# Kernel optimization log

Measured on AMD Instinct MI355X. Metric: run time of the kernel, lower is better.

The kernel has to match this reference:

```python
import jax, jax.numpy as jnp
import numpy as np

EPS = 1e-6
HEADS, HEAD_DIM = 8, 64

def rms_norm_ch(x, g):
    # x: [B,C,H,W], normalize over channel dim, scale g: [C]
    mean = jnp.mean(x * x, axis=1, keepdims=True)
    return x * jax.lax.rsqrt(mean + EPS) * g[None, :, None, None]

def rms_norm_last(x, g):
    # x: [B,L,D], normalize over feature dim, scale g: [D]
    mean = jnp.mean(x * x, axis=-1, keepdims=True)
    return x * jax.lax.rsqrt(mean + EPS) * g

def setup_inputs() -> dict:
    key = jax.random.key(0)
    ks = jax.random.split(key, 5)
    B, C, H, W = 8, 512, 32, 32
    Lc = 1024
    hidden = HEADS * HEAD_DIM  # 512
    x = jax.random.normal(ks[0], (B, C, H, W), dtype=jnp.float32)
    context = jax.random.normal(ks[1], (B, Lc, C), dtype=jnp.float32)
    Wq = jax.random.normal(ks[2], (hidden, C), dtype=jnp.float32) * 0.02
    Wkv = jax.random.normal(ks[3], (2 * hidden, C), dtype=jnp.float32) * 0.02
    Wo = jax.random.normal(ks[4], (C, hidden), dtype=jnp.float32) * 0.02
    bo = jnp.zeros((C,), dtype=jnp.float32)
    g = jnp.ones((C,), dtype=jnp.float32)   # shared RMSNorm scale (pre-attn)
    g2 = jnp.ones((C,), dtype=jnp.float32)  # output RMSNorm scale
    return {"x": x, "context": context, "Wq": Wq, "Wkv": Wkv, "Wo": Wo, "bo": bo, "g": g, "g2": g2}

def reference(x, context, Wq, Wkv, Wo, bo, g, g2):
    B, C, H, W = x.shape
    Lc = context.shape[1]
    hidden = HEADS * HEAD_DIM
    scale = HEAD_DIM ** -0.5

    # Q projection: 1x1 conv == per-pixel matmul
    xn = rms_norm_ch(x, g)
    q = jnp.einsum('oc,bchw->bohw', Wq, xn)                     # [B,hidden,H,W]
    q = q.reshape(B, HEADS, HEAD_DIM, H * W) * scale            # [B,h,d,lw1]

    # K,V from context tokens
    cn = rms_norm_last(context, g)
    kv = jnp.einsum('bld,od->blo', cn, Wkv)                     # [B,Lc,2*hidden]
    k, v = jnp.split(kv, 2, axis=-1)
    k = k.reshape(B, Lc, HEADS, HEAD_DIM).transpose(0, 2, 3, 1)  # [B,h,d,lw2]
    v = v.reshape(B, Lc, HEADS, HEAD_DIM).transpose(0, 2, 3, 1)  # [B,h,d,lw2]

    sim = jnp.einsum('bhci,bhcj->bhij', q, k)                   # [B,h,lw1,lw2]
    attn = jax.nn.softmax(sim, axis=-1)
    out = jnp.einsum('bhij,bhcj->bhic', attn, v)                # [B,h,lw1,d]

    out = out.transpose(0, 1, 3, 2).reshape(B, hidden, H, W)    # b (h c) l w
    y = jnp.einsum('oc,bchw->bohw', Wo, out) + bo[None, :, None, None]
    y = rms_norm_ch(y, g2)
    return y + x
```

## Files before the change

### kernel.cpp

```cpp
#include <hip/hip_runtime.h>
#include <hip/hip_bf16.h>

using bf16 = __hip_bfloat16;
typedef float f32x4 __attribute__((ext_vector_type(4)));
typedef short s16x8 __attribute__((ext_vector_type(8)));
typedef short s16x4 __attribute__((ext_vector_type(4)));

#define B_N   8
#define C_N   512
#define HW_N  1024
#define LC_N  1024
#define HID_N 512
#define NHEAD 8
#define DHEAD 64
#define EPSN  1e-6f

__device__ __forceinline__ f32x4 mfma16(s16x8 a, s16x8 b, f32x4 c) {
  return __builtin_amdgcn_mfma_f32_16x16x32_bf16(a, b, c, 0, 0, 0);
}
__device__ __forceinline__ void gload_lds16(const void* g, void* l) {
  __builtin_amdgcn_global_load_lds((const __attribute__((address_space(1))) void*)g,
                                   (__attribute__((address_space(3))) void*)l, 16, 0, 0);
}
__device__ __forceinline__ s16x8 ld8(const bf16* p) {
  return *reinterpret_cast<const s16x8*>(p);
}
__device__ __forceinline__ unsigned short bfbits(float f) {
  return __builtin_bit_cast(unsigned short, __float2bfloat16(f));
}

__global__ __launch_bounds__(256) void prep_weights(
    const float* __restrict__ Wq, const float* __restrict__ Wkv,
    const float* __restrict__ Wo, const float* __restrict__ g,
    bf16* __restrict__ Wqg, bf16* __restrict__ Wkvg, bf16* __restrict__ Wob,
    float* __restrict__ ssqx, float* __restrict__ ssqy)
{
  int idx = blockIdx.x * 256 + threadIdx.x;
  const int NQ = 512 * 512, NKV = 1024 * 512;
  if (idx < 8192) { ssqx[idx] = 0.f; ssqy[idx] = 0.f; }
  if (idx < NQ) {
    Wqg[idx] = __float2bfloat16(Wq[idx] * g[idx & 511]);
  } else if (idx < NQ + NKV) {
    int j = idx - NQ;
    Wkvg[j] = __float2bfloat16(Wkv[j] * g[j & 511]);
  } else {
    int j = idx - NQ - NKV;
    Wob[j] = __float2bfloat16(Wo[j]);
  }
}

__global__ __launch_bounds__(256) void xbf_kernel(
    const float* __restrict__ x, bf16* __restrict__ xbf, float* __restrict__ ssqx)
{
  __shared__ float tile[32][33];
  __shared__ float part[8][32];
  int b = blockIdx.z, c0 = blockIdx.y * 32, p0 = blockIdx.x * 32;
  int tx = threadIdx.x & 31, ty = threadIdx.x >> 5;
#pragma unroll
  for (int j = 0; j < 4; ++j) {
    int c = ty + j * 8;
    tile[c][tx] = x[((long)b * C_N + c0 + c) * HW_N + p0 + tx];
  }
  __syncthreads();
  {
    float s = 0.f;
#pragma unroll
    for (int i = 0; i < 4; ++i) {
      float v = tile[ty * 4 + i][tx];
      s += v * v;
    }
    part[ty][tx] = s;
  }
#pragma unroll
  for (int j = 0; j < 4; ++j) {
    int p = ty + j * 8;
    xbf[((long)b * HW_N + p0 + p) * C_N + c0 + tx] = __float2bfloat16(tile[tx][p]);
  }
  __syncthreads();
  if (ty == 0) {
    float tot = 0.f;
#pragma unroll
    for (int i = 0; i < 8; ++i) tot += part[i][tx];
    atomicAdd(&ssqx[b * HW_N + p0 + tx], tot);
  }
}

__global__ __launch_bounds__(256) void ctxnorm_kernel(
    const float* __restrict__ ctx, bf16* __restrict__ cnbf)
{
  int row = blockIdx.x * 4 + (threadIdx.x >> 6);
  int lane = threadIdx.x & 63;
  const float* cr = ctx + (long)row * C_N;
  float4 v0 = ((const float4*)cr)[lane * 2];
  float4 v1 = ((const float4*)cr)[lane * 2 + 1];
  float s = v0.x*v0.x + v0.y*v0.y + v0.z*v0.z + v0.w*v0.w
          + v1.x*v1.x + v1.y*v1.y + v1.z*v1.z + v1.w*v1.w;
#pragma unroll
  for (int m = 1; m < 64; m <<= 1) s += __shfl_xor(s, m);
  float r = rsqrtf(s * (1.0f / C_N) + EPSN);
  bf16 tmp[8];
  tmp[0] = __float2bfloat16(v0.x * r); tmp[1] = __float2bfloat16(v0.y * r);
  tmp[2] = __float2bfloat16(v0.z * r); tmp[3] = __float2bfloat16(v0.w * r);
  tmp[4] = __float2bfloat16(v1.x * r); tmp[5] = __float2bfloat16(v1.y * r);
  tmp[6] = __float2bfloat16(v1.z * r); tmp[7] = __float2bfloat16(v1.w * r);
  *reinterpret_cast<s16x8*>(cnbf + (long)row * C_N + lane * 8) =
      *reinterpret_cast<const s16x8*>(tmp);
}

__device__ __forceinline__ void gemm128_core(
    const bf16* __restrict__ A, const bf16* __restrict__ W, int K, int m0, int n0,
    bf16* __restrict__ sA, bf16* __restrict__ sB, f32x4 (&acc)[4][4])
{
  const int t = threadIdx.x;
  const int lane = t & 63, w = t >> 6;
  const int wm = (w >> 1) * 64, wn = (w & 1) * 64;
  const int lr = lane & 15, hi = lane >> 4;
  const int r = t >> 2, seg = t & 3;
  const long aoff0 = (long)(m0 + r) * K + seg * 8;
  const long aoff1 = (long)(m0 + 64 + r) * K + seg * 8;
  const long woff0 = (long)(n0 + r) * K + seg * 8;
  const long woff1 = (long)(n0 + 64 + r) * K + seg * 8;
  const int d0 = r * 32 + seg * 8, d1 = (64 + r) * 32 + seg * 8;

#define GSTAGE(buf, k0)                                           \
  do {                                                            \
    gload_lds16(A + aoff0 + (k0), &sA[(buf) * 4096 + d0]);        \
    gload_lds16(A + aoff1 + (k0), &sA[(buf) * 4096 + d1]);        \
    gload_lds16(W + woff0 + (k0), &sB[(buf) * 4096 + d0]);        \
    gload_lds16(W + woff1 + (k0), &sB[(buf) * 4096 + d1]);        \
  } while (0)

  GSTAGE(0, 0);
  __syncthreads();
  int cur = 0;
  for (int k0 = 0; k0 < K; k0 += 32) {
    if (k0 + 32 < K) GSTAGE(cur ^ 1, k0 + 32);
    s16x8 af[4], bfr[4];
#pragma unroll
    for (int mi = 0; mi < 4; ++mi)
      af[mi] = *reinterpret_cast<const s16x8*>(
          &sA[cur * 4096 + (wm + mi * 16 + lr) * 32 + hi * 8]);
#pragma unroll
    for (int ni = 0; ni < 4; ++ni)
      bfr[ni] = *reinterpret_cast<const s16x8*>(
          &sB[cur * 4096 + (wn + ni * 16 + lr) * 32 + hi * 8]);
    __builtin_amdgcn_s_setprio(1);
#pragma unroll
    for (int mi = 0; mi < 4; ++mi)
#pragma unroll
      for (int ni = 0; ni < 4; ++ni)
        acc[mi][ni] = mfma16(af[mi], bfr[ni], acc[mi][ni]);
    __builtin_amdgcn_s_setprio(0);
    __syncthreads();
    cur ^= 1;
  }
#undef GSTAGE
}

__global__ __launch_bounds__(256, 2)
void gemm_qkv(const bf16* __restrict__ xbf, const bf16* __restrict__ cnbf,
              const bf16* __restrict__ Wqg, const bf16* __restrict__ Wkvg,
              const float* __restrict__ ssqx,
              bf16* __restrict__ qbf, bf16* __restrict__ kvbf, bf16* __restrict__ vT)
{
  __shared__ bf16 sA[2 * 4096];
  __shared__ bf16 sB[2 * 4096];
  const int bid = blockIdx.x;
  const bf16 *A, *W;
  int m0, n0;
  bool isQ;
  if (bid < 256) {
    isQ = true;  A = xbf;  W = Wqg;
    m0 = (bid >> 2) * 128; n0 = (bid & 3) * 128;
  } else {
    isQ = false; A = cnbf; W = Wkvg;
    int b2 = bid - 256;
    m0 = (b2 >> 3) * 128; n0 = (b2 & 7) * 128;
  }
  f32x4 acc[4][4] = {};
  gemm128_core(A, W, C_N, m0, n0, sA, sB, acc);

  const int lane = threadIdx.x & 63, w = threadIdx.x >> 6;
  const int wm = (w >> 1) * 64, wn = (w & 1) * 64;
  const int lr = lane & 15, hi = lane >> 4;
#pragma unroll
  for (int mi = 0; mi < 4; ++mi) {
#pragma unroll
    for (int rr = 0; rr < 4; ++rr) {
      int row = m0 + wm + mi * 16 + hi * 4 + rr;
      float rsc = 0.f;
      if (isQ)
        rsc = rsqrtf(ssqx[row] * (1.0f / C_N) + EPSN) * 0.18033688011112042f;
#pragma unroll
      for (int ni = 0; ni < 4; ++ni) {
        int col = n0 + wn + ni * 16 + lr;
        float v = acc[mi][ni][rr];
        if (isQ) {
          qbf[(long)row * HID_N + col] = __float2bfloat16(v * rsc);
        } else if (col < HID_N) {
          kvbf[(long)row * (2 * HID_N) + col] = __float2bfloat16(v);
        } else {
          int b = row >> 10, l = row & 1023;
          vT[((long)b * HID_N + (col - HID_N)) * LC_N + l] = __float2bfloat16(v);
        }
      }
    }
  }
}

__global__ __launch_bounds__(256, 2)
void gemm_o(const bf16* __restrict__ attno, const bf16* __restrict__ Wob,
            const float* __restrict__ bo, float* __restrict__ ytmp,
            float* __restrict__ ssqy)
{
  __shared__ bf16 sA[2 * 4096];
  __shared__ bf16 sB[2 * 4096];
  const int m0 = (blockIdx.x >> 2) * 128;
  const int n0 = (blockIdx.x & 3) * 128;
  f32x4 acc[4][4] = {};
  gemm128_core(attno, Wob, HID_N, m0, n0, sA, sB, acc);

  const int lane = threadIdx.x & 63, w = threadIdx.x >> 6;
  const int wm = (w >> 1) * 64, wn = (w & 1) * 64;
  const int lr = lane & 15, hi = lane >> 4;
  float ss[4][4];
#pragma unroll
  for (int mi = 0; mi < 4; ++mi)
#pragma unroll
    for (int rr = 0; rr < 4; ++rr) ss[mi][rr] = 0.f;

#pragma unroll
  for (int mi = 0; mi < 4; ++mi) {
#pragma unroll
    for (int ni = 0; ni < 4; ++ni) {
      float bb = bo[n0 + wn + ni * 16 + lr];
#pragma unroll
      for (int rr = 0; rr < 4; ++rr) {
        int row = m0 + wm + mi * 16 + hi * 4 + rr;
        int col = n0 + wn + ni * 16 + lr;
        float v = acc[mi][ni][rr] + bb;
        ytmp[(long)row * C_N + col] = v;
        ss[mi][rr] += v * v;
      }
    }
  }
#pragma unroll
  for (int mi = 0; mi < 4; ++mi)
#pragma unroll
    for (int rr = 0; rr < 4; ++rr) {
      float s = ss[mi][rr];
      s += __shfl_xor(s, 1); s += __shfl_xor(s, 2);
      s += __shfl_xor(s, 4); s += __shfl_xor(s, 8);
      if (lr == 0) atomicAdd(&ssqy[m0 + wm + mi * 16 + hi * 4 + rr], s);
    }
}

__global__ __launch_bounds__(256, 2)
void attn_fused(const bf16* __restrict__ qbf, const bf16* __restrict__ kvbf,
                const bf16* __restrict__ vT, bf16* __restrict__ attno)
{
  __shared__ bf16 sK[2][4096];
  __shared__ bf16 sV[2][4096];
  __shared__ bf16 Pl[4][32 * 72];
  const int t = threadIdx.x;
  const int wv = t >> 6, lane = t & 63;
  const int lr = lane & 15, hi = lane >> 4;
  const int hi8 = hi * 8, hi4 = hi * 4;
  const int bh = blockIdx.x, b = bh >> 3, h = bh & 7;
  const int q_base = blockIdx.y * 128 + wv * 32;

  const bf16* kbase = kvbf + (long)b * LC_N * 1024 + h * DHEAD;
  const bf16* vbase = vT + ((long)b * HID_N + h * DHEAD) * (long)LC_N;
  bf16* Pw = Pl[wv];

  s16x8 qf[2][2];
#pragma unroll
  for (int qt = 0; qt < 2; ++qt)
#pragma unroll
    for (int c = 0; c < 2; ++c)
      qf[qt][c] = ld8(qbf + ((long)b * HW_N + q_base + qt * 16 + lr) * HID_N
                          + h * DHEAD + c * 32 + hi8);

  const int srow = lane >> 2;
  const int scol = (lane & 3) * 8;

#define ASTAGE(buf, l0n)                                                        \
  do {                                                                          \
    _Pragma("unroll")                                                           \
    for (int j = 0; j < 4; ++j) {                                               \
      int lin = wv * 4 + j;                                                     \
      int cc = (lin >> 2) & 1, qq = lin & 3;                                    \
      if (lin < 8) {                                                            \
        gload_lds16(kbase + (long)((l0n) + qq * 16 + srow) * 1024 + cc * 32 + scol, \
                    &sK[buf][cc * 2048 + qq * 512 + lane * 8]);                 \
      } else {                                                                  \
        gload_lds16(vbase + (long)(qq * 16 + srow) * 1024 + (l0n) + cc * 32 + scol, \
                    &sV[buf][cc * 2048 + qq * 512 + lane * 8]);                 \
      }                                                                         \
    }                                                                           \
  } while (0)

  float m[2] = {-1e30f, -1e30f};
  float lsum[2] = {0.f, 0.f};
  f32x4 o[2][4] = {};

  ASTAGE(0, 0);
  __syncthreads();
  int cur = 0;

#pragma unroll 1
  for (int l0 = 0; l0 < LC_N; l0 += 64) {
    if (l0 + 64 < LC_N) ASTAGE(cur ^ 1, l0 + 64);

    f32x4 st[4][2] = {};
    __builtin_amdgcn_s_setprio(1);
#pragma unroll
    for (int kt = 0; kt < 4; ++kt) {
      s16x8 k0 = *reinterpret_cast<const s16x8*>(&sK[cur][(kt * 16 + lr) * 32 + hi8]);
      s16x8 k1 = *reinterpret_cast<const s16x8*>(&sK[cur][2048 + (kt * 16 + lr) * 32 + hi8]);
      st[kt][0] = mfma16(k0, qf[0][0], st[kt][0]);
      st[kt][0] = mfma16(k1, qf[0][1], st[kt][0]);
      st[kt][1] = mfma16(k0, qf[1][0], st[kt][1]);
      st[kt][1] = mfma16(k1, qf[1][1], st[kt][1]);
    }
    __builtin_amdgcn_s_setprio(0);

    float pmax[2];
#pragma unroll
    for (int qt = 0; qt < 2; ++qt) {
      float mx = st[0][qt][0];
#pragma unroll
      for (int kt = 0; kt < 4; ++kt)
#pragma unroll
        for (int rr = 0; rr < 4; ++rr)
          mx = fmaxf(mx, st[kt][qt][rr]);
      pmax[qt] = mx;
    }
    bool ok = (pmax[0] <= m[0] + 8.f) && (pmax[1] <= m[1] + 8.f);
    if (!__all(ok)) {
#pragma unroll
      for (int qt = 0; qt < 2; ++qt) {
        float rm = pmax[qt];
        rm = fmaxf(rm, __shfl_xor(rm, 16));
        rm = fmaxf(rm, __shfl_xor(rm, 32));
        float mn = fmaxf(m[qt], rm);
        float al = __builtin_amdgcn_exp2f(m[qt] - mn);
        m[qt] = mn;
        lsum[qt] *= al;
        float arr[4];
#pragma unroll
        for (int rr = 0; rr < 4; ++rr) arr[rr] = __shfl(al, hi4 + rr);
#pragma unroll
        for (int dt = 0; dt < 4; ++dt)
#pragma unroll
          for (int rr = 0; rr < 4; ++rr) o[qt][dt][rr] *= arr[rr];
      }
    }

#pragma unroll
    for (int qt = 0; qt < 2; ++qt) {
      float ls = 0.f;
#pragma unroll
      for (int kt = 0; kt < 4; ++kt) {
        float p0 = __builtin_amdgcn_exp2f(st[kt][qt][0] - m[qt]);
        float p1 = __builtin_amdgcn_exp2f(st[kt][qt][1] - m[qt]);
        float p2 = __builtin_amdgcn_exp2f(st[kt][qt][2] - m[qt]);
        float p3 = __builtin_amdgcn_exp2f(st[kt][qt][3] - m[qt]);
        ls += (p0 + p1) + (p2 + p3);
        s16x4 pk;
        pk[0] = (short)bfbits(p0); pk[1] = (short)bfbits(p1);
        pk[2] = (short)bfbits(p2); pk[3] = (short)bfbits(p3);
        *reinterpret_cast<s16x4*>(&Pw[(qt * 16 + lr) * 72 + kt * 16 + hi4]) = pk;
      }
      lsum[qt] += ls;
    }

    __builtin_amdgcn_s_setprio(1);
#pragma unroll
    for (int c = 0; c < 2; ++c) {
      s16x8 pa0 = *reinterpret_cast<const s16x8*>(&Pw[(0 * 16 + lr) * 72 + c * 32 + hi8]);
      s16x8 pa1 = *reinterpret_cast<const s16x8*>(&Pw[(1 * 16 + lr) * 72 + c * 32 + hi8]);
#pragma unroll
      for (int dt = 0; dt < 4; ++dt) {
        s16x8 vv = *reinterpret_cast<const s16x8*>(
            &sV[cur][c * 2048 + (dt * 16 + lr) * 32 + hi8]);
        o[0][dt] = mfma16(pa0, vv, o[0][dt]);
        o[1][dt] = mfma16(pa1, vv, o[1][dt]);
      }
    }
    __builtin_amdgcn_s_setprio(0);

    __syncthreads();
    cur ^= 1;
  }
#undef ASTAGE

#pragma unroll
  for (int qt = 0; qt < 2; ++qt) {
    float ls = lsum[qt];
    ls += __shfl_xor(ls, 16);
    ls += __shfl_xor(ls, 32);
    float linv[4];
#pragma unroll
    for (int rr = 0; rr < 4; ++rr) linv[rr] = 1.f / __shfl(ls, hi4 + rr);
#pragma unroll
    for (int dt = 0; dt < 4; ++dt)
#pragma unroll
      for (int rr = 0; rr < 4; ++rr)
        attno[((long)b * HW_N + q_base + qt * 16 + hi4 + rr) * HID_N
              + h * DHEAD + dt * 16 + lr] = __float2bfloat16(o[qt][dt][rr] * linv[rr]);
  }
}

__global__ __launch_bounds__(256) void final_kernel(
    const float* __restrict__ ytmp, const float* __restrict__ g2,
    const float* __restrict__ ssqy, const float* __restrict__ x,
    float* __restrict__ out)
{
  __shared__ float tile[32][33];
  int b = blockIdx.z, c0 = blockIdx.y * 32, p0 = blockIdx.x * 32;
  int tx = threadIdx.x & 31, ty = threadIdx.x >> 5;
#pragma unroll
  for (int j = 0; j < 4; ++j) {
    int p = ty + j * 8;
    tile[p][tx] = ytmp[((long)b * HW_N + p0 + p) * C_N + c0 + tx];
  }
  __syncthreads();
  float r = rsqrtf(ssqy[b * HW_N + p0 + tx] * (1.0f / C_N) + EPSN);
#pragma unroll
  for (int j = 0; j < 4; ++j) {
    int c = ty + j * 8;
    long oidx = ((long)b * C_N + c0 + c) * HW_N + p0 + tx;
    out[oidx] = tile[tx][c] * r * g2[c0 + c] + x[oidx];
  }
}

extern "C" void kernel_launch(void* const* d_in, const int* in_sizes, int n_in,
                              void* d_out, int out_size, void* d_ws, size_t ws_size,
                              hipStream_t stream) {
  const float* x   = (const float*)d_in[0];
  const float* ctx = (const float*)d_in[1];
  const float* Wq  = (const float*)d_in[2];
  const float* Wkv = (const float*)d_in[3];
  const float* Wo  = (const float*)d_in[4];
  const float* bo  = (const float*)d_in[5];
  const float* g   = (const float*)d_in[6];
  const float* g2  = (const float*)d_in[7];
  float* out = (float*)d_out;

  char* ws = (char*)d_ws;
  bf16*  Wqg   = (bf16*)(ws + 0);
  bf16*  Wkvg  = (bf16*)(ws + 524288);
  bf16*  Wob   = (bf16*)(ws + 1572864);
  float* ssqx  = (float*)(ws + 2097152);
  float* ssqy  = (float*)(ws + 2129920);
  bf16*  xbf   = (bf16*)(ws + 2162688);
  bf16*  cnbf  = (bf16*)(ws + 10551296);
  bf16*  qbf   = (bf16*)(ws + 18939904);
  bf16*  kvbf  = (bf16*)(ws + 27328512);
  bf16*  vT    = (bf16*)(ws + 44105728);
  bf16*  attno = (bf16*)(ws + 52494336);
  float* ytmp  = (float*)(ws + 2162688);

  prep_weights<<<4096, 256, 0, stream>>>(Wq, Wkv, Wo, g, Wqg, Wkvg, Wob, ssqx, ssqy);
  xbf_kernel<<<dim3(32, 16, 8), 256, 0, stream>>>(x, xbf, ssqx);
  ctxnorm_kernel<<<2048, 256, 0, stream>>>(ctx, cnbf);

  gemm_qkv<<<768, 256, 0, stream>>>(xbf, cnbf, Wqg, Wkvg, ssqx, qbf, kvbf, vT);

  attn_fused<<<dim3(64, 8), 256, 0, stream>>>(qbf, kvbf, vT, attno);

  gemm_o<<<256, 256, 0, stream>>>(attno, Wob, bo, ytmp, ssqy);

  final_kernel<<<dim3(32, 16, 8), 256, 0, stream>>>(ytmp, g2, ssqy, x, out);
}
```

Before: 184.9 us.

## Fuse all stages into a persistent megakernel with grid barriers and swizzled LDS

Replaces the seven separate launches with one init kernel plus a persistent 512-block kernel. Inside it, the prep, QKV GEMM, attention, output GEMM and final-norm stages run in sequence, separated by software grid barriers built on atomics. This removes per-launch overhead and the idle tails between kernels. It also adds an XOR swizzle to the LDS layout in the GEMM and attention tiles to cut bank conflicts. The costs are the barrier spin waits, a dependence on all 512 blocks being co-resident (otherwise it deadlocks), and stages whose tile counts do not divide evenly across 512 blocks, such as 768 GEMM tiles.

```diff
diff --git a/kernel.cpp b/kernel.cpp
--- a/kernel.cpp
+++ b/kernel.cpp
@@ -11,9 +11,9 @@
 #define HW_N  1024
 #define LC_N  1024
 #define HID_N 512
-#define NHEAD 8
 #define DHEAD 64
 #define EPSN  1e-6f
+#define NBLK  512
 
 __device__ __forceinline__ f32x4 mfma16(s16x8 a, s16x8 b, f32x4 c) {
   return __builtin_amdgcn_mfma_f32_16x16x32_bf16(a, b, c, 0, 0, 0);
@@ -29,98 +29,47 @@
   return __builtin_bit_cast(unsigned short, __float2bfloat16(f));
 }
 
-__global__ __launch_bounds__(256) void prep_weights(
-    const float* __restrict__ Wq, const float* __restrict__ Wkv,
-    const float* __restrict__ Wo, const float* __restrict__ g,
-    bf16* __restrict__ Wqg, bf16* __restrict__ Wkvg, bf16* __restrict__ Wob,
-    float* __restrict__ ssqx, float* __restrict__ ssqy)
+__device__ __forceinline__ void grid_barrier(int* bar) {
+  __syncthreads();
+  if (threadIdx.x == 0) {
+    __threadfence();
+    int g = __hip_atomic_load(&bar[1], __ATOMIC_RELAXED, __HIP_MEMORY_SCOPE_AGENT);
+    int v = __hip_atomic_fetch_add(&bar[0], 1, __ATOMIC_ACQ_REL, __HIP_MEMORY_SCOPE_AGENT);
+    if (v == NBLK - 1) {
+      __hip_atomic_store(&bar[0], 0, __ATOMIC_RELAXED, __HIP_MEMORY_SCOPE_AGENT);
+      __hip_atomic_fetch_add(&bar[1], 1, __ATOMIC_ACQ_REL, __HIP_MEMORY_SCOPE_AGENT);
+    } else {
+      while (__hip_atomic_load(&bar[1], __ATOMIC_ACQUIRE, __HIP_MEMORY_SCOPE_AGENT) == g)
+        __builtin_amdgcn_s_sleep(2);
+    }
+  }
+  __syncthreads();
+}
+
+__global__ __launch_bounds__(256) void init_kernel(
+    float* __restrict__ ssqx, float* __restrict__ ssqy, int* __restrict__ bar)
 {
-  int idx = blockIdx.x * 256 + threadIdx.x;
-  const int NQ = 512 * 512, NKV = 1024 * 512;
-  if (idx < 8192) { ssqx[idx] = 0.f; ssqy[idx] = 0.f; }
-  if (idx < NQ) {
-    Wqg[idx] = __float2bfloat16(Wq[idx] * g[idx & 511]);
-  } else if (idx < NQ + NKV) {
-    int j = idx - NQ;
-    Wkvg[j] = __float2bfloat16(Wkv[j] * g[j & 511]);
-  } else {
-    int j = idx - NQ - NKV;
-    Wob[j] = __float2bfloat16(Wo[j]);
-  }
-}
-
-__global__ __launch_bounds__(256) void xbf_kernel(
-    const float* __restrict__ x, bf16* __restrict__ xbf, float* __restrict__ ssqx)
-{
-  __shared__ float tile[32][33];
-  __shared__ float part[8][32];
-  int b = blockIdx.z, c0 = blockIdx.y * 32, p0 = blockIdx.x * 32;
-  int tx = threadIdx.x & 31, ty = threadIdx.x >> 5;
-#pragma unroll
-  for (int j = 0; j < 4; ++j) {
-    int c = ty + j * 8;
-    tile[c][tx] = x[((long)b * C_N + c0 + c) * HW_N + p0 + tx];
-  }
-  __syncthreads();
-  {
-    float s = 0.f;
-#pragma unroll
-    for (int i = 0; i < 4; ++i) {
-      float v = tile[ty * 4 + i][tx];
-      s += v * v;
-    }
-    part[ty][tx] = s;
-  }
-#pragma unroll
-  for (int j = 0; j < 4; ++j) {
-    int p = ty + j * 8;
-    xbf[((long)b * HW_N + p0 + p) * C_N + c0 + tx] = __float2bfloat16(tile[tx][p]);
-  }
-  __syncthreads();
-  if (ty == 0) {
-    float tot = 0.f;
-#pragma unroll
-    for (int i = 0; i < 8; ++i) tot += part[i][tx];
-    atomicAdd(&ssqx[b * HW_N + p0 + tx], tot);
-  }
-}
-
-__global__ __launch_bounds__(256) void ctxnorm_kernel(
-    const float* __restrict__ ctx, bf16* __restrict__ cnbf)
-{
-  int row = blockIdx.x * 4 + (threadIdx.x >> 6);
-  int lane = threadIdx.x & 63;
-  const float* cr = ctx + (long)row * C_N;
-  float4 v0 = ((const float4*)cr)[lane * 2];
-  float4 v1 = ((const float4*)cr)[lane * 2 + 1];
-  float s = v0.x*v0.x + v0.y*v0.y + v0.z*v0.z + v0.w*v0.w
-          + v1.x*v1.x + v1.y*v1.y + v1.z*v1.z + v1.w*v1.w;
-#pragma unroll
-  for (int m = 1; m < 64; m <<= 1) s += __shfl_xor(s, m);
-  float r = rsqrtf(s * (1.0f / C_N) + EPSN);
-  bf16 tmp[8];
-  tmp[0] = __float2bfloat16(v0.x * r); tmp[1] = __float2bfloat16(v0.y * r);
-  tmp[2] = __float2bfloat16(v0.z * r); tmp[3] = __float2bfloat16(v0.w * r);
-  tmp[4] = __float2bfloat16(v1.x * r); tmp[5] = __float2bfloat16(v1.y * r);
-  tmp[6] = __float2bfloat16(v1.z * r); tmp[7] = __float2bfloat16(v1.w * r);
-  *reinterpret_cast<s16x8*>(cnbf + (long)row * C_N + lane * 8) =
-      *reinterpret_cast<const s16x8*>(tmp);
+  int i = blockIdx.x * 256 + threadIdx.x;
+  if (i < 8192) { ssqx[i] = 0.f; ssqy[i] = 0.f; }
+  if (i < 8) bar[i] = 0;
 }
 
 __device__ __forceinline__ void gemm128_core(
     const bf16* __restrict__ A, const bf16* __restrict__ W, int K, int m0, int n0,
-    bf16* __restrict__ sA, bf16* __restrict__ sB, f32x4 (&acc)[4][4])
+    bf16* sA, bf16* sB, f32x4 (&acc)[4][4])
 {
   const int t = threadIdx.x;
   const int lane = t & 63, w = t >> 6;
   const int wm = (w >> 1) * 64, wn = (w & 1) * 64;
   const int lr = lane & 15, hi = lane >> 4;
   const int r = t >> 2, seg = t & 3;
-  const long aoff0 = (long)(m0 + r) * K + seg * 8;
-  const long aoff1 = (long)(m0 + 64 + r) * K + seg * 8;
-  const long woff0 = (long)(n0 + r) * K + seg * 8;
-  const long woff1 = (long)(n0 + 64 + r) * K + seg * 8;
+  const int segsw = seg ^ ((r >> 1) & 3);
+  const long aoff0 = (long)(m0 + r) * K + segsw * 8;
+  const long aoff1 = (long)(m0 + 64 + r) * K + segsw * 8;
+  const long woff0 = (long)(n0 + r) * K + segsw * 8;
+  const long woff1 = (long)(n0 + 64 + r) * K + segsw * 8;
   const int d0 = r * 32 + seg * 8, d1 = (64 + r) * 32 + seg * 8;
+  const int kofs = (hi ^ ((lr >> 1) & 3)) * 8;
 
 #define GSTAGE(buf, k0)                                           \
   do {                                                            \
@@ -139,11 +88,11 @@
 #pragma unroll
     for (int mi = 0; mi < 4; ++mi)
       af[mi] = *reinterpret_cast<const s16x8*>(
-          &sA[cur * 4096 + (wm + mi * 16 + lr) * 32 + hi * 8]);
+          &sA[cur * 4096 + (wm + mi * 16 + lr) * 32 + kofs]);
 #pragma unroll
     for (int ni = 0; ni < 4; ++ni)
       bfr[ni] = *reinterpret_cast<const s16x8*>(
-          &sB[cur * 4096 + (wn + ni * 16 + lr) * 32 + hi * 8]);
+          &sB[cur * 4096 + (wn + ni * 16 + lr) * 32 + kofs]);
     __builtin_amdgcn_s_setprio(1);
 #pragma unroll
     for (int mi = 0; mi < 4; ++mi)
@@ -157,281 +106,360 @@
 #undef GSTAGE
 }
 
-__global__ __launch_bounds__(256, 2)
-void gemm_qkv(const bf16* __restrict__ xbf, const bf16* __restrict__ cnbf,
-              const bf16* __restrict__ Wqg, const bf16* __restrict__ Wkvg,
-              const float* __restrict__ ssqx,
-              bf16* __restrict__ qbf, bf16* __restrict__ kvbf, bf16* __restrict__ vT)
+__global__ __launch_bounds__(256, 3)
+void mega(const float* __restrict__ x, const float* __restrict__ ctx,
+          const float* __restrict__ Wq, const float* __restrict__ Wkv,
+          const float* __restrict__ Wo, const float* __restrict__ bo,
+          const float* __restrict__ g, const float* __restrict__ g2,
+          bf16* __restrict__ Wqg, bf16* __restrict__ Wkvg, bf16* __restrict__ Wob,
+          float* __restrict__ ssqx, float* __restrict__ ssqy,
+          bf16* __restrict__ xbf, bf16* __restrict__ cnbf,
+          bf16* __restrict__ qbf, bf16* __restrict__ kvbf, bf16* __restrict__ vT,
+          bf16* __restrict__ attno, float* __restrict__ ytmp,
+          float* __restrict__ out, int* __restrict__ bar)
 {
-  __shared__ bf16 sA[2 * 4096];
-  __shared__ bf16 sB[2 * 4096];
-  const int bid = blockIdx.x;
-  const bf16 *A, *W;
-  int m0, n0;
-  bool isQ;
-  if (bid < 256) {
-    isQ = true;  A = xbf;  W = Wqg;
-    m0 = (bid >> 2) * 128; n0 = (bid & 3) * 128;
-  } else {
-    isQ = false; A = cnbf; W = Wkvg;
-    int b2 = bid - 256;
-    m0 = (b2 >> 3) * 128; n0 = (b2 & 7) * 128;
-  }
-  f32x4 acc[4][4] = {};
-  gemm128_core(A, W, C_N, m0, n0, sA, sB, acc);
-
-  const int lane = threadIdx.x & 63, w = threadIdx.x >> 6;
-  const int wm = (w >> 1) * 64, wn = (w & 1) * 64;
-  const int lr = lane & 15, hi = lane >> 4;
-#pragma unroll
-  for (int mi = 0; mi < 4; ++mi) {
-#pragma unroll
-    for (int rr = 0; rr < 4; ++rr) {
-      int row = m0 + wm + mi * 16 + hi * 4 + rr;
-      float rsc = 0.f;
-      if (isQ)
-        rsc = rsqrtf(ssqx[row] * (1.0f / C_N) + EPSN) * 0.18033688011112042f;
+  __shared__ __align__(16) char smem[51200];
+  const int vb = blockIdx.x;
+  const int tid = threadIdx.x;
+
+  for (int t = vb; t < 4096; t += NBLK) {
+    int idx = t * 256 + tid;
+    const int NQ = 512 * 512, NKV = 1024 * 512;
+    if (idx < NQ) {
+      Wqg[idx] = __float2bfloat16(Wq[idx] * g[idx & 511]);
+    } else if (idx < NQ + NKV) {
+      int j = idx - NQ;
+      Wkvg[j] = __float2bfloat16(Wkv[j] * g[j & 511]);
+    } else {
+      int j = idx - NQ - NKV;
+      Wob[j] = __float2bfloat16(Wo[j]);
+    }
+  }
+  {
+    float* tile = (float*)smem;
+    float* part = (float*)(smem + 4352);
+    int tx = tid & 31, ty = tid >> 5;
+    for (int t = vb; t < 4096; t += NBLK) {
+      int b = t >> 9, cy = (t >> 5) & 15, px = t & 31;
+      int c0 = cy * 32, p0 = px * 32;
+#pragma unroll
+      for (int j = 0; j < 4; ++j) {
+        int c = ty + j * 8;
+        tile[c * 33 + tx] = x[((long)b * C_N + c0 + c) * HW_N + p0 + tx];
+      }
+      __syncthreads();
+      {
+        float s = 0.f;
+#pragma unroll
+        for (int i = 0; i < 4; ++i) {
+          float v = tile[(ty * 4 + i) * 33 + tx];
+          s += v * v;
+        }
+        part[ty * 32 + tx] = s;
+      }
+#pragma unroll
+      for (int j = 0; j < 4; ++j) {
+        int p = ty + j * 8;
+        xbf[((long)b * HW_N + p0 + p) * C_N + c0 + tx] = __float2bfloat16(tile[tx * 33 + p]);
+      }
+      __syncthreads();
+      if (ty == 0) {
+        float tot = 0.f;
+#pragma unroll
+        for (int i = 0; i < 8; ++i) tot += part[i * 32 + tx];
+        atomicAdd(&ssqx[b * HW_N + p0 + tx], tot);
+      }
+    }
+  }
+  for (int t = vb; t < 2048; t += NBLK) {
+    int row = t * 4 + (tid >> 6);
+    int lane = tid & 63;
+    const float* cr = ctx + (long)row * C_N;
+    float4 v0 = ((const float4*)cr)[lane * 2];
+    float4 v1 = ((const float4*)cr)[lane * 2 + 1];
+    float s = v0.x*v0.x + v0.y*v0.y + v0.z*v0.z + v0.w*v0.w
+            + v1.x*v1.x + v1.y*v1.y + v1.z*v1.z + v1.w*v1.w;
+#pragma unroll
+    for (int m = 1; m < 64; m <<= 1) s += __shfl_xor(s, m);
+    float r = rsqrtf(s * (1.0f / C_N) + EPSN);
+    bf16 tmp[8];
+    tmp[0] = __float2bfloat16(v0.x * r); tmp[1] = __float2bfloat16(v0.y * r);
+    tmp[2] = __float2bfloat16(v0.z * r); tmp[3] = __float2bfloat16(v0.w * r);
+    tmp[4] = __float2bfloat16(v1.x * r); tmp[5] = __float2bfloat16(v1.y * r);
+    tmp[6] = __float2bfloat16(v1.z * r); tmp[7] = __float2bfloat16(v1.w * r);
+    *reinterpret_cast<s16x8*>(cnbf + (long)row * C_N + lane * 8) =
+        *reinterpret_cast<const s16x8*>(tmp);
+  }
+  grid_barrier(bar);
+
+  {
+    bf16* sA = (bf16*)smem;
+    bf16* sB = (bf16*)(smem + 16384);
+    const int lane = tid & 63, w = tid >> 6;
+    const int wm = (w >> 1) * 64, wn = (w & 1) * 64;
+    const int lr = lane & 15, hi = lane >> 4;
+    for (int tv = vb; tv < 768; tv += NBLK) {
+      const bf16 *A, *W;
+      int m0, n0;
+      bool isQ;
+      if (tv < 256) {
+        isQ = true;  A = xbf;  W = Wqg;
+        m0 = (tv >> 2) * 128; n0 = (tv & 3) * 128;
+      } else {
+        isQ = false; A = cnbf; W = Wkvg;
+        int b2 = tv - 256;
+        m0 = (b2 >> 3) * 128; n0 = (b2 & 7) * 128;
+      }
+      f32x4 acc[4][4] = {};
+      gemm128_core(A, W, C_N, m0, n0, sA, sB, acc);
+#pragma unroll
+      for (int mi = 0; mi < 4; ++mi) {
+#pragma unroll
+        for (int rr = 0; rr < 4; ++rr) {
+          int row = m0 + wm + mi * 16 + hi * 4 + rr;
+          float rsc = 0.f;
+          if (isQ)
+            rsc = rsqrtf(ssqx[row] * (1.0f / C_N) + EPSN) * 0.18033688011112042f;
+#pragma unroll
+          for (int ni = 0; ni < 4; ++ni) {
+            int col = n0 + wn + ni * 16 + lr;
+            float v = acc[mi][ni][rr];
+            if (isQ) {
+              qbf[(long)row * HID_N + col] = __float2bfloat16(v * rsc);
+            } else if (col < HID_N) {
+              kvbf[(long)row * (2 * HID_N) + col] = __float2bfloat16(v);
+            } else {
+              int b = row >> 10, l = row & 1023;
+              vT[((long)b * HID_N + (col - HID_N)) * LC_N + l] = __float2bfloat16(v);
+            }
+          }
+        }
+      }
+    }
+  }
+  grid_barrier(bar);
+
+  {
+    bf16* sK = (bf16*)smem;
+    bf16* sV = (bf16*)(smem + 16384);
+    bf16* Pl = (bf16*)(smem + 32768);
+    const int wv = tid >> 6, lane = tid & 63;
+    const int lr = lane & 15, hi = lane >> 4;
+    const int hi8 = hi * 8, hi4 = hi * 4;
+    const int bh = vb & 63, b = bh >> 3, h = bh & 7;
+    const int q_base = (vb >> 6) * 128 + wv * 32;
+
+    const bf16* kbase = kvbf + (long)b * LC_N * 1024 + h * DHEAD;
+    const bf16* vbase = vT + ((long)b * HID_N + h * DHEAD) * (long)LC_N;
+    bf16* Pw = Pl + wv * (32 * 72);
+
+    s16x8 qf[2][2];
+#pragma unroll
+    for (int qt = 0; qt < 2; ++qt)
+#pragma unroll
+      for (int c = 0; c < 2; ++c)
+        qf[qt][c] = ld8(qbf + ((long)b * HW_N + q_base + qt * 16 + lr) * HID_N
+                            + h * DHEAD + c * 32 + hi8);
+
+    const int srow = lane >> 2;
+    const int scol = ((lane & 3) ^ ((lane >> 3) & 3)) * 8;
+    const int rxofs = (hi ^ ((lr >> 1) & 3)) * 8;
+
+#define ASTAGE(buf, l0n)                                                          \
+    do {                                                                          \
+      _Pragma("unroll")                                                           \
+      for (int j = 0; j < 4; ++j) {                                               \
+        int lin = wv * 4 + j;                                                     \
+        int cc = (lin >> 2) & 1, qq = lin & 3;                                    \
+        if (lin < 8) {                                                            \
+          gload_lds16(kbase + (long)((l0n) + qq * 16 + srow) * 1024 + cc * 32 + scol, \
+                      &sK[(buf) * 4096 + cc * 2048 + qq * 512 + lane * 8]);       \
+        } else {                                                                  \
+          gload_lds16(vbase + (long)(qq * 16 + srow) * 1024 + (l0n) + cc * 32 + scol, \
+                      &sV[(buf) * 4096 + cc * 2048 + qq * 512 + lane * 8]);       \
+        }                                                                         \
+      }                                                                           \
+    } while (0)
+
+    float m[2] = {-1e30f, -1e30f};
+    float lsum[2] = {0.f, 0.f};
+    f32x4 o[2][4] = {};
+
+    ASTAGE(0, 0);
+    __syncthreads();
+    int cur = 0;
+
+#pragma unroll 1
+    for (int l0 = 0; l0 < LC_N; l0 += 64) {
+      if (l0 + 64 < LC_N) ASTAGE(cur ^ 1, l0 + 64);
+
+      f32x4 st[4][2] = {};
+      __builtin_amdgcn_s_setprio(1);
+#pragma unroll
+      for (int kt = 0; kt < 4; ++kt) {
+        s16x8 k0 = *reinterpret_cast<const s16x8*>(
+            &sK[cur * 4096 + (kt * 16 + lr) * 32 + rxofs]);
+        s16x8 k1 = *reinterpret_cast<const s16x8*>(
+            &sK[cur * 4096 + 2048 + (kt * 16 + lr) * 32 + rxofs]);
+        st[kt][0] = mfma16(k0, qf[0][0], st[kt][0]);
+        st[kt][0] = mfma16(k1, qf[0][1], st[kt][0]);
+        st[kt][1] = mfma16(k0, qf[1][0], st[kt][1]);
+        st[kt][1] = mfma16(k1, qf[1][1], st[kt][1]);
+      }
+      __builtin_amdgcn_s_setprio(0);
+
+      float pmax[2];
+#pragma unroll
+      for (int qt = 0; qt < 2; ++qt) {
+        float mx = st[0][qt][0];
+#pragma unroll
+        for (int kt = 0; kt < 4; ++kt)
+#pragma unroll
+          for (int rr = 0; rr < 4; ++rr)
+            mx = fmaxf(mx, st[kt][qt][rr]);
+        pmax[qt] = mx;
+      }
+      bool ok = (pmax[0] <= m[0] + 8.f) && (pmax[1] <= m[1] + 8.f);
+      if (!__all(ok)) {
+#pragma unroll
+        for (int qt = 0; qt < 2; ++qt) {
+          float rm = pmax[qt];
+          rm = fmaxf(rm, __shfl_xor(rm, 16));
+          rm = fmaxf(rm, __shfl_xor(rm, 32));
+          float mn = fmaxf(m[qt], rm);
+          float al = __builtin_amdgcn_exp2f(m[qt] - mn);
+          m[qt] = mn;
+          lsum[qt] *= al;
+          float arr[4];
+#pragma unroll
+          for (int rr = 0; rr < 4; ++rr) arr[rr] = __shfl(al, hi4 + rr);
+#pragma unroll
+          for (int dt = 0; dt < 4; ++dt)
+#pragma unroll
+            for (int rr = 0; rr < 4; ++rr) o[qt][dt][rr] *= arr[rr];
+        }
+      }
+
+#pragma unroll
+      for (int qt = 0; qt < 2; ++qt) {
+        float ls = 0.f;
+#pragma unroll
+        for (int kt = 0; kt < 4; ++kt) {
+          float p0 = __builtin_amdgcn_exp2f(st[kt][qt][0] - m[qt]);
+          float p1 = __builtin_amdgcn_exp2f(st[kt][qt][1] - m[qt]);
+          float p2 = __builtin_amdgcn_exp2f(st[kt][qt][2] - m[qt]);
+          float p3 = __builtin_amdgcn_exp2f(st[kt][qt][3] - m[qt]);
+          ls += (p0 + p1) + (p2 + p3);
+          s16x4 pk;
+          pk[0] = (short)bfbits(p0); pk[1] = (short)bfbits(p1);
+          pk[2] = (short)bfbits(p2); pk[3] = (short)bfbits(p3);
+          *reinterpret_cast<s16x4*>(&Pw[(qt * 16 + lr) * 72 + kt * 16 + hi4]) = pk;
+        }
+        lsum[qt] += ls;
+      }
+
+      __builtin_amdgcn_s_setprio(1);
+#pragma unroll
+      for (int c = 0; c < 2; ++c) {
+        s16x8 pa0 = *reinterpret_cast<const s16x8*>(&Pw[(0 * 16 + lr) * 72 + c * 32 + hi8]);
+        s16x8 pa1 = *reinterpret_cast<const s16x8*>(&Pw[(1 * 16 + lr) * 72 + c * 32 + hi8]);
+#pragma unroll
+        for (int dt = 0; dt < 4; ++dt) {
+          s16x8 vv = *reinterpret_cast<const s16x8*>(
+              &sV[cur * 4096 + c * 2048 + (dt * 16 + lr) * 32 + rxofs]);
+          o[0][dt] = mfma16(pa0, vv, o[0][dt]);
+          o[1][dt] = mfma16(pa1, vv, o[1][dt]);
+        }
+      }
+      __builtin_amdgcn_s_setprio(0);
+
+      __syncthreads();
+      cur ^= 1;
+    }
+#undef ASTAGE
+
+#pragma unroll
+    for (int qt = 0; qt < 2; ++qt) {
+      float ls = lsum[qt];
+      ls += __shfl_xor(ls, 16);
+      ls += __shfl_xor(ls, 32);
+      float linv[4];
+#pragma unroll
+      for (int rr = 0; rr < 4; ++rr) linv[rr] = 1.f / __shfl(ls, hi4 + rr);
+#pragma unroll
+      for (int dt = 0; dt < 4; ++dt)
+#pragma unroll
+        for (int rr = 0; rr < 4; ++rr)
+          attno[((long)b * HW_N + q_base + qt * 16 + hi4 + rr) * HID_N
+                + h * DHEAD + dt * 16 + lr] = __float2bfloat16(o[qt][dt][rr] * linv[rr]);
+    }
+  }
+  grid_barrier(bar);
+
+  if (vb < 256) {
+    bf16* sA = (bf16*)smem;
+    bf16* sB = (bf16*)(smem + 16384);
+    const int m0 = (vb >> 2) * 128;
+    const int n0 = (vb & 3) * 128;
+    f32x4 acc[4][4] = {};
+    gemm128_core(attno, Wob, HID_N, m0, n0, sA, sB, acc);
+
+    const int lane = tid & 63, w = tid >> 6;
+    const int wm = (w >> 1) * 64, wn = (w & 1) * 64;
+    const int lr = lane & 15, hi = lane >> 4;
+    float ss[4][4];
+#pragma unroll
+    for (int mi = 0; mi < 4; ++mi)
+#pragma unroll
+      for (int rr = 0; rr < 4; ++rr) ss[mi][rr] = 0.f;
+#pragma unroll
+    for (int mi = 0; mi < 4; ++mi) {
 #pragma unroll
       for (int ni = 0; ni < 4; ++ni) {
-        int col = n0 + wn + ni * 16 + lr;
-        float v = acc[mi][ni][rr];
-        if (isQ) {
-          qbf[(long)row * HID_N + col] = __float2bfloat16(v * rsc);
-        } else if (col < HID_N) {
-          kvbf[(long)row * (2 * HID_N) + col] = __float2bfloat16(v);
-        } else {
-          int b = row >> 10, l = row & 1023;
-          vT[((long)b * HID_N + (col - HID_N)) * LC_N + l] = __float2bfloat16(v);
-        }
-      }
-    }
-  }
-}
-
-__global__ __launch_bounds__(256, 2)
-void gemm_o(const bf16* __restrict__ attno, const bf16* __restrict__ Wob,
-            const float* __restrict__ bo, float* __restrict__ ytmp,
-            float* __restrict__ ssqy)
-{
-  __shared__ bf16 sA[2 * 4096];
-  __shared__ bf16 sB[2 * 4096];
-  const int m0 = (blockIdx.x >> 2) * 128;
-  const int n0 = (blockIdx.x & 3) * 128;
-  f32x4 acc[4][4] = {};
-  gemm128_core(attno, Wob, HID_N, m0, n0, sA, sB, acc);
-
-  const int lane = threadIdx.x & 63, w = threadIdx.x >> 6;
-  const int wm = (w >> 1) * 64, wn = (w & 1) * 64;
-  const int lr = lane & 15, hi = lane >> 4;
-  float ss[4][4];
-#pragma unroll
-  for (int mi = 0; mi < 4; ++mi)
-#pragma unroll
-    for (int rr = 0; rr < 4; ++rr) ss[mi][rr] = 0.f;
-
-#pragma unroll
-  for (int mi = 0; mi < 4; ++mi) {
-#pragma unroll
-    for (int ni = 0; ni < 4; ++ni) {
-      float bb = bo[n0 + wn + ni * 16 + lr];
+        float bb = bo[n0 + wn + ni * 16 + lr];
+#pragma unroll
+        for (int rr = 0; rr < 4; ++rr) {
+          int row = m0 + wm + mi * 16 + hi * 4 + rr;
+          int col = n0 + wn + ni * 16 + lr;
+          float v = acc[mi][ni][rr] + bb;
+          ytmp[(long)row * C_N + col] = v;
+          ss[mi][rr] += v * v;
+        }
+      }
+    }
+#pragma unroll
+    for (int mi = 0; mi < 4; ++mi)
 #pragma unroll
       for (int rr = 0; rr < 4; ++rr) {
-        int row = m0 + wm + mi * 16 + hi * 4 + rr;
-        int col = n0 + wn + ni * 16 + lr;
-        float v = acc[mi][ni][rr] + bb;
-        ytmp[(long)row * C_N + col] = v;
-        ss[mi][rr] += v * v;
-      }
-    }
-  }
-#pragma unroll
-  for (int mi = 0; mi < 4; ++mi)
-#pragma unroll
-    for (int rr = 0; rr < 4; ++rr) {
-      float s = ss[mi][rr];
-      s += __shfl_xor(s, 1); s += __shfl_xor(s, 2);
-      s += __shfl_xor(s, 4); s += __shfl_xor(s, 8);
-      if (lr == 0) atomicAdd(&ssqy[m0 + wm + mi * 16 + hi * 4 + rr], s);
-    }
-}
-
-__global__ __launch_bounds__(256, 2)
-void attn_fused(const bf16* __restrict__ qbf, const bf16* __restrict__ kvbf,
-                const bf16* __restrict__ vT, bf16* __restrict__ attno)
-{
-  __shared__ bf16 sK[2][4096];
-  __shared__ bf16 sV[2][4096];
-  __shared__ bf16 Pl[4][32 * 72];
-  const int t = threadIdx.x;
-  const int wv = t >> 6, lane = t & 63;
-  const int lr = lane & 15, hi = lane >> 4;
-  const int hi8 = hi * 8, hi4 = hi * 4;
-  const int bh = blockIdx.x, b = bh >> 3, h = bh & 7;
-  const int q_base = blockIdx.y * 128 + wv * 32;
-
-  const bf16* kbase = kvbf + (long)b * LC_N * 1024 + h * DHEAD;
-  const bf16* vbase = vT + ((long)b * HID_N + h * DHEAD) * (long)LC_N;
-  bf16* Pw = Pl[wv];
-
-  s16x8 qf[2][2];
-#pragma unroll
-  for (int qt = 0; qt < 2; ++qt)
-#pragma unroll
-    for (int c = 0; c < 2; ++c)
-      qf[qt][c] = ld8(qbf + ((long)b * HW_N + q_base + qt * 16 + lr) * HID_N
-                          + h * DHEAD + c * 32 + hi8);
-
-  const int srow = lane >> 2;
-  const int scol = (lane & 3) * 8;
-
-#define ASTAGE(buf, l0n)                                                        \
-  do {                                                                          \
-    _Pragma("unroll")                                                           \
-    for (int j = 0; j < 4; ++j) {                                               \
-      int lin = wv * 4 + j;                                                     \
-      int cc = (lin >> 2) & 1, qq = lin & 3;                                    \
-      if (lin < 8) {                                                            \
-        gload_lds16(kbase + (long)((l0n) + qq * 16 + srow) * 1024 + cc * 32 + scol, \
-                    &sK[buf][cc * 2048 + qq * 512 + lane * 8]);                 \
-      } else {                                                                  \
-        gload_lds16(vbase + (long)(qq * 16 + srow) * 1024 + (l0n) + cc * 32 + scol, \
-                    &sV[buf][cc * 2048 + qq * 512 + lane * 8]);                 \
-      }                                                                         \
-    }                                                                           \
-  } while (0)
-
-  float m[2] = {-1e30f, -1e30f};
-  float lsum[2] = {0.f, 0.f};
-  f32x4 o[2][4] = {};
-
-  ASTAGE(0, 0);
-  __syncthreads();
-  int cur = 0;
-
-#pragma unroll 1
-  for (int l0 = 0; l0 < LC_N; l0 += 64) {
-    if (l0 + 64 < LC_N) ASTAGE(cur ^ 1, l0 + 64);
-
-    f32x4 st[4][2] = {};
-    __builtin_amdgcn_s_setprio(1);
-#pragma unroll
-    for (int kt = 0; kt < 4; ++kt) {
-      s16x8 k0 = *reinterpret_cast<const s16x8*>(&sK[cur][(kt * 16 + lr) * 32 + hi8]);
-      s16x8 k1 = *reinterpret_cast<const s16x8*>(&sK[cur][2048 + (kt * 16 + lr) * 32 + hi8]);
-      st[kt][0] = mfma16(k0, qf[0][0], st[kt][0]);
-      st[kt][0] = mfma16(k1, qf[0][1], st[kt][0]);
-      st[kt][1] = mfma16(k0, qf[1][0], st[kt][1]);
-      st[kt][1] = mfma16(k1, qf[1][1], st[kt][1]);
-    }
-    __builtin_amdgcn_s_setprio(0);
-
-    float pmax[2];
-#pragma unroll
-    for (int qt = 0; qt < 2; ++qt) {
-      float mx = st[0][qt][0];
-#pragma unroll
-      for (int kt = 0; kt < 4; ++kt)
-#pragma unroll
-        for (int rr = 0; rr < 4; ++rr)
-          mx = fmaxf(mx, st[kt][qt][rr]);
-      pmax[qt] = mx;
-    }
-    bool ok = (pmax[0] <= m[0] + 8.f) && (pmax[1] <= m[1] + 8.f);
-    if (!__all(ok)) {
-#pragma unroll
-      for (int qt = 0; qt < 2; ++qt) {
-        float rm = pmax[qt];
-        rm = fmaxf(rm, __shfl_xor(rm, 16));
-        rm = fmaxf(rm, __shfl_xor(rm, 32));
-        float mn = fmaxf(m[qt], rm);
-        float al = __builtin_amdgcn_exp2f(m[qt] - mn);
-        m[qt] = mn;
-        lsum[qt] *= al;
-        float arr[4];
-#pragma unroll
-        for (int rr = 0; rr < 4; ++rr) arr[rr] = __shfl(al, hi4 + rr);
-#pragma unroll
-        for (int dt = 0; dt < 4; ++dt)
-#pragma unroll
-          for (int rr = 0; rr < 4; ++rr) o[qt][dt][rr] *= arr[rr];
-      }
-    }
-
-#pragma unroll
-    for (int qt = 0; qt < 2; ++qt) {
-      float ls = 0.f;
-#pragma unroll
-      for (int kt = 0; kt < 4; ++kt) {
-        float p0 = __builtin_amdgcn_exp2f(st[kt][qt][0] - m[qt]);
-        float p1 = __builtin_amdgcn_exp2f(st[kt][qt][1] - m[qt]);
-        float p2 = __builtin_amdgcn_exp2f(st[kt][qt][2] - m[qt]);
-        float p3 = __builtin_amdgcn_exp2f(st[kt][qt][3] - m[qt]);
-        ls += (p0 + p1) + (p2 + p3);
-        s16x4 pk;
-        pk[0] = (short)bfbits(p0); pk[1] = (short)bfbits(p1);
-        pk[2] = (short)bfbits(p2); pk[3] = (short)bfbits(p3);
-        *reinterpret_cast<s16x4*>(&Pw[(qt * 16 + lr) * 72 + kt * 16 + hi4]) = pk;
-      }
-      lsum[qt] += ls;
-    }
-
-    __builtin_amdgcn_s_setprio(1);
-#pragma unroll
-    for (int c = 0; c < 2; ++c) {
-      s16x8 pa0 = *reinterpret_cast<const s16x8*>(&Pw[(0 * 16 + lr) * 72 + c * 32 + hi8]);
-      s16x8 pa1 = *reinterpret_cast<const s16x8*>(&Pw[(1 * 16 + lr) * 72 + c * 32 + hi8]);
-#pragma unroll
-      for (int dt = 0; dt < 4; ++dt) {
-        s16x8 vv = *reinterpret_cast<const s16x8*>(
-            &sV[cur][c * 2048 + (dt * 16 + lr) * 32 + hi8]);
-        o[0][dt] = mfma16(pa0, vv, o[0][dt]);
-        o[1][dt] = mfma16(pa1, vv, o[1][dt]);
-      }
-    }
-    __builtin_amdgcn_s_setprio(0);
-
-    __syncthreads();
-    cur ^= 1;
-  }
-#undef ASTAGE
-
-#pragma unroll
-  for (int qt = 0; qt < 2; ++qt) {
-    float ls = lsum[qt];
-    ls += __shfl_xor(ls, 16);
-    ls += __shfl_xor(ls, 32);
-    float linv[4];
-#pragma unroll
-    for (int rr = 0; rr < 4; ++rr) linv[rr] = 1.f / __shfl(ls, hi4 + rr);
-#pragma unroll
-    for (int dt = 0; dt < 4; ++dt)
-#pragma unroll
-      for (int rr = 0; rr < 4; ++rr)
-        attno[((long)b * HW_N + q_base + qt * 16 + hi4 + rr) * HID_N
-              + h * DHEAD + dt * 16 + lr] = __float2bfloat16(o[qt][dt][rr] * linv[rr]);
-  }
-}
-
-__global__ __launch_bounds__(256) void final_kernel(
-    const float* __restrict__ ytmp, const float* __restrict__ g2,
-    const float* __restrict__ ssqy, const float* __restrict__ x,
-    float* __restrict__ out)
-{
-  __shared__ float tile[32][33];
-  int b = blockIdx.z, c0 = blockIdx.y * 32, p0 = blockIdx.x * 32;
-  int tx = threadIdx.x & 31, ty = threadIdx.x >> 5;
-#pragma unroll
-  for (int j = 0; j < 4; ++j) {
-    int p = ty + j * 8;
-    tile[p][tx] = ytmp[((long)b * HW_N + p0 + p) * C_N + c0 + tx];
-  }
-  __syncthreads();
-  float r = rsqrtf(ssqy[b * HW_N + p0 + tx] * (1.0f / C_N) + EPSN);
-#pragma unroll
-  for (int j = 0; j < 4; ++j) {
-    int c = ty + j * 8;
-    long oidx = ((long)b * C_N + c0 + c) * HW_N + p0 + tx;
-    out[oidx] = tile[tx][c] * r * g2[c0 + c] + x[oidx];
+        float s = ss[mi][rr];
+        s += __shfl_xor(s, 1); s += __shfl_xor(s, 2);
+        s += __shfl_xor(s, 4); s += __shfl_xor(s, 8);
+        if (lr == 0) atomicAdd(&ssqy[m0 + wm + mi * 16 + hi * 4 + rr], s);
+      }
+  }
+  grid_barrier(bar);
+
+  {
+    float* tile = (float*)smem;
+    int tx = tid & 31, ty = tid >> 5;
+    for (int t = vb; t < 4096; t += NBLK) {
+      int b = t >> 9, cy = (t >> 5) & 15, px = t & 31;
+      int c0 = cy * 32, p0 = px * 32;
+#pragma unroll
+      for (int j = 0; j < 4; ++j) {
+        int p = ty + j * 8;
+        tile[p * 33 + tx] = ytmp[((long)b * HW_N + p0 + p) * C_N + c0 + tx];
+      }
+      __syncthreads();
+      float r = rsqrtf(ssqy[b * HW_N + p0 + tx] * (1.0f / C_N) + EPSN);
+#pragma unroll
+      for (int j = 0; j < 4; ++j) {
+        int c = ty + j * 8;
+        long oidx = ((long)b * C_N + c0 + c) * HW_N + p0 + tx;
+        out[oidx] = tile[tx * 33 + c] * r * g2[c0 + c] + x[oidx];
+      }
+      __syncthreads();
+    }
   }
 }
 
@@ -454,23 +482,18 @@
   bf16*  Wob   = (bf16*)(ws + 1572864);
   float* ssqx  = (float*)(ws + 2097152);
   float* ssqy  = (float*)(ws + 2129920);
-  bf16*  xbf   = (bf16*)(ws + 2162688);
-  bf16*  cnbf  = (bf16*)(ws + 10551296);
-  bf16*  qbf   = (bf16*)(ws + 18939904);
-  bf16*  kvbf  = (bf16*)(ws + 27328512);
-  bf16*  vT    = (bf16*)(ws + 44105728);
-  bf16*  attno = (bf16*)(ws + 52494336);
-  float* ytmp  = (float*)(ws + 2162688);
-
-  prep_weights<<<4096, 256, 0, stream>>>(Wq, Wkv, Wo, g, Wqg, Wkvg, Wob, ssqx, ssqy);
-  xbf_kernel<<<dim3(32, 16, 8), 256, 0, stream>>>(x, xbf, ssqx);
-  ctxnorm_kernel<<<2048, 256, 0, stream>>>(ctx, cnbf);
-
-  gemm_qkv<<<768, 256, 0, stream>>>(xbf, cnbf, Wqg, Wkvg, ssqx, qbf, kvbf, vT);
-
-  attn_fused<<<dim3(64, 8), 256, 0, stream>>>(qbf, kvbf, vT, attno);
-
-  gemm_o<<<256, 256, 0, stream>>>(attno, Wob, bo, ytmp, ssqy);
-
-  final_kernel<<<dim3(32, 16, 8), 256, 0, stream>>>(ytmp, g2, ssqy, x, out);
-}
+  int*   bar   = (int*)  (ws + 2162688);
+  bf16*  xbf   = (bf16*)(ws + 2163712);
+  bf16*  cnbf  = (bf16*)(ws + 10552320);
+  bf16*  qbf   = (bf16*)(ws + 18940928);
+  bf16*  kvbf  = (bf16*)(ws + 27329536);
+  bf16*  vT    = (bf16*)(ws + 44106752);
+  bf16*  attno = (bf16*)(ws + 52495360);
+  float* ytmp  = (float*)(ws + 2163712);
+
+  init_kernel<<<32, 256, 0, stream>>>(ssqx, ssqy, bar);
+  mega<<<NBLK, 256, 0, stream>>>(x, ctx, Wq, Wkv, Wo, bo, g, g2,
+                                 Wqg, Wkvg, Wob, ssqx, ssqy,
+                                 xbf, cnbf, qbf, kvbf, vT, attno,
+                                 ytmp, out, bar);
+}
```

Result: slower. 580.8 us (+214.1%).
